# Kernel optimization log

Hardware: AMD Instinct MI355X
Metric: run time of the kernel (lower is better)

The kernel has to match this reference:

```python
import jax, jax.numpy as jnp
import numpy as np

LMAX = 3

def make_i2l(lmax):
    # [(lmax+1)^2, lmax+1] 0/1 indicator mapping irrep index -> degree l
    i2l = np.zeros(((lmax + 1) ** 2, lmax + 1), dtype=np.float32)
    count = 0
    for l in range(lmax + 1):
        i2l[count:count + 2 * l + 1, l] = 1.0
        count += 2 * l + 1
    return jnp.asarray(i2l)

def setup_inputs() -> dict:
    key = jax.random.key(0)
    x = jax.random.normal(key, (32, 512, 16, 128), dtype=jnp.float32)  # [b, n, irrep, c]
    i2l = make_i2l(LMAX)
    return {"x": x, "i2l": i2l}

def reference(x, i2l):
    # degree-wise squared norm per neighbor: [b, n, l, c]
    dot = x * x
    ll2 = jnp.einsum('bnic,il->bnlc', dot, i2l)
    # argmax over neighbors, keepdim -> [b, 1, l, c]
    idx = jnp.argmax(ll2, axis=1, keepdims=True)
    # broadcast degree-wise winner index back to irrep components: [b, 1, irrep, c]
    idx_i = jnp.einsum('belc,il->beic', idx.astype(x.dtype), i2l).astype(jnp.int32)
    # gather winning neighbor per (irrep, channel), squeeze neighbor dim -> [b, irrep, c]
    out = jnp.take_along_axis(x, idx_i, axis=1)[:, 0]
    return out
```

## Files before the change

kernel.cpp:

```cpp
#include <hip/hip_runtime.h>
#include <stdint.h>


constexpr int B_  = 32;
constexpr int N_  = 512;
constexpr int IR_ = 16;
constexpr int C_  = 128;
constexpr int NL_ = 4;

constexpr int NCHUNK = 32;
constexpr int CHN    = N_ / NCHUNK;
constexpr int NROW   = 4;
constexpr int NN     = CHN / NROW;

__device__ constexpr int L_OF_I[16] = {0, 1,1,1, 2,2,2,2,2, 3,3,3,3,3,3,3};

__global__ __launch_bounds__(128)
void cmp_phase1(const float* __restrict__ x, unsigned long long* __restrict__ ws) {
    const int t    = threadIdx.x;
    const int c4   = t & 31;
    const int nrow = t >> 5;
    const int chunk = blockIdx.x;
    const int b     = blockIdx.y;

    unsigned long long best[NL_][4];
#pragma unroll
    for (int l = 0; l < NL_; ++l)
#pragma unroll
        for (int j = 0; j < 4; ++j) best[l][j] = 0ull;

    const int n0 = chunk * CHN + nrow * NN;
    const float4* __restrict__ x4 = (const float4*)x;

    for (int nn = 0; nn < NN; ++nn) {
        const int n = n0 + nn;
        const long base = ((long)(b * N_ + n) * IR_) * 32 + c4;

        float4 acc[NL_];
#pragma unroll
        for (int l = 0; l < NL_; ++l) { acc[l].x = acc[l].y = acc[l].z = acc[l].w = 0.f; }

#pragma unroll
        for (int i = 0; i < IR_; ++i) {
            const float4 v = x4[base + i * 32];
            const int l = L_OF_I[i];
            acc[l].x += v.x * v.x;
            acc[l].y += v.y * v.y;
            acc[l].z += v.z * v.z;
            acc[l].w += v.w * v.w;
        }

        const unsigned long long code = (unsigned long long)(~(unsigned int)n);
#pragma unroll
        for (int l = 0; l < NL_; ++l) {
            const float vals[4] = {acc[l].x, acc[l].y, acc[l].z, acc[l].w};
#pragma unroll
            for (int j = 0; j < 4; ++j) {
                const unsigned long long p =
                    ((unsigned long long)__float_as_uint(vals[j]) << 32) | code;
                if (p > best[l][j]) best[l][j] = p;
            }
        }
    }

    __shared__ unsigned long long red[NROW][NL_ * C_];
#pragma unroll
    for (int l = 0; l < NL_; ++l)
#pragma unroll
        for (int j = 0; j < 4; ++j)
            red[nrow][l * C_ + c4 * 4 + j] = best[l][j];
    __syncthreads();

#pragma unroll
    for (int k = 0; k < 4; ++k) {
        const int e = t + k * 128;
        unsigned long long m = red[0][e];
#pragma unroll
        for (int nr = 1; nr < NROW; ++nr) {
            const unsigned long long v = red[nr][e];
            if (v > m) m = v;
        }
        atomicMax(&ws[(long)b * (NL_ * C_) + e], m);
    }
}

__global__ __launch_bounds__(128)
void cmp_phase2(const float* __restrict__ x,
                const unsigned long long* __restrict__ ws,
                float* __restrict__ out) {
    const int c = threadIdx.x;
    const int b = blockIdx.x;

    int n_l[NL_];
#pragma unroll
    for (int l = 0; l < NL_; ++l) {
        const unsigned long long p = ws[(long)b * (NL_ * C_) + l * C_ + c];
        n_l[l] = (int)(~(unsigned int)(p & 0xFFFFFFFFull));
    }

#pragma unroll
    for (int i = 0; i < IR_; ++i) {
        const int n = n_l[L_OF_I[i]];
        out[((long)b * IR_ + i) * C_ + c] = x[(((long)b * N_ + n) * IR_ + i) * C_ + c];
    }
}

extern "C" void kernel_launch(void* const* d_in, const int* in_sizes, int n_in,
                              void* d_out, int out_size, void* d_ws, size_t ws_size,
                              hipStream_t stream) {
    const float* x = (const float*)d_in[0];
    unsigned long long* ws = (unsigned long long*)d_ws;
    float* out = (float*)d_out;

    hipMemsetAsync(d_ws, 0, (size_t)B_ * NL_ * C_ * sizeof(unsigned long long), stream);

    dim3 g1(NCHUNK, B_);
    cmp_phase1<<<g1, 128, 0, stream>>>(x, ws);
    cmp_phase2<<<B_, 128, 0, stream>>>(x, ws, out);
}
```

Before: 191.0 us.

## Replace global atomicMax and memset with per-chunk partials reduced in phase2

Phase1 now writes each chunk's packed (value,index) maxima to its own slice of the workspace instead of doing global atomicMax, so the hipMemsetAsync launch is no longer needed. Phase2 is split over (batch, degree) blocks, reduces the 32 chunk partials per element, and copies only the irreps belonging to that degree. The inner neighbor loop of phase1 is also fully unrolled. In exchange, the workspace grows by a factor of 32 and phase2 must read all of those partials.

```diff
diff --git a/kernel.cpp b/kernel.cpp
--- a/kernel.cpp
+++ b/kernel.cpp
@@ -7,6 +7,7 @@
 constexpr int IR_ = 16;
 constexpr int C_  = 128;
 constexpr int NL_ = 4;
+constexpr int E_  = NL_ * C_;
 
 constexpr int NCHUNK = 32;
 constexpr int CHN    = N_ / NCHUNK;
@@ -14,6 +15,8 @@
 constexpr int NN     = CHN / NROW;
 
 __device__ constexpr int L_OF_I[16] = {0, 1,1,1, 2,2,2,2,2, 3,3,3,3,3,3,3};
+__device__ constexpr int I0_OF_L[4] = {0, 1, 4, 9};
+__device__ constexpr int NI_OF_L[4] = {1, 3, 5, 7};
 
 __global__ __launch_bounds__(128)
 void cmp_phase1(const float* __restrict__ x, unsigned long long* __restrict__ ws) {
@@ -32,6 +35,7 @@
     const int n0 = chunk * CHN + nrow * NN;
     const float4* __restrict__ x4 = (const float4*)x;
 
+#pragma unroll
     for (int nn = 0; nn < NN; ++nn) {
         const int n = n0 + nn;
         const long base = ((long)(b * N_ + n) * IR_) * 32 + c4;
@@ -63,7 +67,7 @@
         }
     }
 
-    __shared__ unsigned long long red[NROW][NL_ * C_];
+    __shared__ unsigned long long red[NROW][E_];
 #pragma unroll
     for (int l = 0; l < NL_; ++l)
 #pragma unroll
@@ -71,6 +75,7 @@
             red[nrow][l * C_ + c4 * 4 + j] = best[l][j];
     __syncthreads();
 
+    unsigned long long* __restrict__ wsp = ws + ((long)chunk * B_ + b) * E_;
 #pragma unroll
     for (int k = 0; k < 4; ++k) {
         const int e = t + k * 128;
@@ -80,7 +85,7 @@
             const unsigned long long v = red[nr][e];
             if (v > m) m = v;
         }
-        atomicMax(&ws[(long)b * (NL_ * C_) + e], m);
+        wsp[e] = m;
     }
 }
 
@@ -90,18 +95,24 @@
                 float* __restrict__ out) {
     const int c = threadIdx.x;
     const int b = blockIdx.x;
+    const int l = blockIdx.y;
+    const int e = l * C_ + c;
 
-    int n_l[NL_];
+    unsigned long long m = 0ull;
 #pragma unroll
-    for (int l = 0; l < NL_; ++l) {
-        const unsigned long long p = ws[(long)b * (NL_ * C_) + l * C_ + c];
-        n_l[l] = (int)(~(unsigned int)(p & 0xFFFFFFFFull));
+    for (int chunk = 0; chunk < NCHUNK; ++chunk) {
+        const unsigned long long v = ws[((long)chunk * B_ + b) * E_ + e];
+        if (v > m) m = v;
     }
+    const int n = (int)(~(unsigned int)(m & 0xFFFFFFFFull));
 
-#pragma unroll
-    for (int i = 0; i < IR_; ++i) {
-        const int n = n_l[L_OF_I[i]];
-        out[((long)b * IR_ + i) * C_ + c] = x[(((long)b * N_ + n) * IR_ + i) * C_ + c];
+    const int i0 = I0_OF_L[l];
+    const int ni = NI_OF_L[l];
+    const long src = (((long)b * N_ + n) * IR_ + i0) * C_ + c;
+    const long dst = ((long)b * IR_ + i0) * C_ + c;
+#pragma unroll 7
+    for (int k = 0; k < ni; ++k) {
+        out[dst + (long)k * C_] = x[src + (long)k * C_];
     }
 }
 
@@ -112,9 +123,8 @@
     unsigned long long* ws = (unsigned long long*)d_ws;
     float* out = (float*)d_out;
 
-    hipMemsetAsync(d_ws, 0, (size_t)B_ * NL_ * C_ * sizeof(unsigned long long), stream);
-
     dim3 g1(NCHUNK, B_);
     cmp_phase1<<<g1, 128, 0, stream>>>(x, ws);
-    cmp_phase2<<<B_, 128, 0, stream>>>(x, ws, out);
+    dim3 g2(B_, NL_);
+    cmp_phase2<<<g2, 128, 0, stream>>>(x, ws, out);
 }
```

New measurement: 188.8 us, median of 2. Within noise of the previous version (-1.1%).

## Fuse argmax and gather into one kernel split by channel groups

Applied to the files above, without the earlier changes.

Replaces the memset plus two-kernel scheme (partial argmax with global atomicMax, then gather) with one kernel per (batch, 16-channel group). Each block scans all 512 neighbors for its channels, reduces with wave shuffles and shared memory, then gathers the winners directly. This removes the memset, the atomics and the second launch. The cost is that each thread now reads only a 64-byte contiguous slice per row, so global reads are less coalesced, and the grid is 256 blocks.

```diff
diff --git a/kernel.cpp b/kernel.cpp
--- a/kernel.cpp
+++ b/kernel.cpp
@@ -8,20 +8,24 @@
 constexpr int C_  = 128;
 constexpr int NL_ = 4;
 
-constexpr int NCHUNK = 32;
-constexpr int CHN    = N_ / NCHUNK;
-constexpr int NROW   = 4;
-constexpr int NN     = CHN / NROW;
+constexpr int CG_ = 8;
+constexpr int CW_ = C_ / CG_;
+constexpr int NROW = 64;
+constexpr int KN   = N_ / NROW;
 
 __device__ constexpr int L_OF_I[16] = {0, 1,1,1, 2,2,2,2,2, 3,3,3,3,3,3,3};
 
-__global__ __launch_bounds__(128)
-void cmp_phase1(const float* __restrict__ x, unsigned long long* __restrict__ ws) {
+__global__ __launch_bounds__(256)
+void cmp_fused(const float* __restrict__ x, float* __restrict__ out) {
     const int t    = threadIdx.x;
-    const int c4   = t & 31;
-    const int nrow = t >> 5;
-    const int chunk = blockIdx.x;
-    const int b     = blockIdx.y;
+    const int c4   = t & 3;
+    const int nrow = t >> 2;
+    const int wv   = t >> 6;
+    const int b    = blockIdx.x;
+    const int cg   = blockIdx.y;
+
+    const unsigned colf4 = (unsigned)(cg * 4 + c4);
+    const float4* __restrict__ x4 = (const float4*)x;
 
     unsigned long long best[NL_][4];
 #pragma unroll
@@ -29,12 +33,9 @@
 #pragma unroll
         for (int j = 0; j < 4; ++j) best[l][j] = 0ull;
 
-    const int n0 = chunk * CHN + nrow * NN;
-    const float4* __restrict__ x4 = (const float4*)x;
-
-    for (int nn = 0; nn < NN; ++nn) {
-        const int n = n0 + nn;
-        const long base = ((long)(b * N_ + n) * IR_) * 32 + c4;
+    for (int k = 0; k < KN; ++k) {
+        const int n = nrow + k * NROW;
+        const unsigned base = ((unsigned)(b * N_ + n) * IR_) * 32u + colf4;
 
         float4 acc[NL_];
 #pragma unroll
@@ -63,58 +64,53 @@
         }
     }
 
-    __shared__ unsigned long long red[NROW][NL_ * C_];
 #pragma unroll
     for (int l = 0; l < NL_; ++l)
 #pragma unroll
-        for (int j = 0; j < 4; ++j)
-            red[nrow][l * C_ + c4 * 4 + j] = best[l][j];
+        for (int j = 0; j < 4; ++j) {
+#pragma unroll
+            for (int m = 4; m < 64; m <<= 1) {
+                const unsigned long long q = __shfl_xor(best[l][j], m, 64);
+                if (q > best[l][j]) best[l][j] = q;
+            }
+        }
+
+    __shared__ unsigned long long red[4][NL_ * CW_];
+    __shared__ int nwin[NL_ * CW_];
+    if ((t & 63) < 4) {
+#pragma unroll
+        for (int l = 0; l < NL_; ++l)
+#pragma unroll
+            for (int j = 0; j < 4; ++j)
+                red[wv][l * CW_ + c4 * 4 + j] = best[l][j];
+    }
     __syncthreads();
 
+    if (t < NL_ * CW_) {
+        unsigned long long m = red[0][t];
 #pragma unroll
-    for (int k = 0; k < 4; ++k) {
-        const int e = t + k * 128;
-        unsigned long long m = red[0][e];
-#pragma unroll
-        for (int nr = 1; nr < NROW; ++nr) {
-            const unsigned long long v = red[nr][e];
+        for (int w = 1; w < 4; ++w) {
+            const unsigned long long v = red[w][t];
             if (v > m) m = v;
         }
-        atomicMax(&ws[(long)b * (NL_ * C_) + e], m);
+        nwin[t] = (int)(~(unsigned int)(m & 0xFFFFFFFFull));
     }
-}
+    __syncthreads();
 
-__global__ __launch_bounds__(128)
-void cmp_phase2(const float* __restrict__ x,
-                const unsigned long long* __restrict__ ws,
-                float* __restrict__ out) {
-    const int c = threadIdx.x;
-    const int b = blockIdx.x;
-
-    int n_l[NL_];
-#pragma unroll
-    for (int l = 0; l < NL_; ++l) {
-        const unsigned long long p = ws[(long)b * (NL_ * C_) + l * C_ + c];
-        n_l[l] = (int)(~(unsigned int)(p & 0xFFFFFFFFull));
-    }
-
-#pragma unroll
-    for (int i = 0; i < IR_; ++i) {
-        const int n = n_l[L_OF_I[i]];
-        out[((long)b * IR_ + i) * C_ + c] = x[(((long)b * N_ + n) * IR_ + i) * C_ + c];
-    }
+    const int i  = t >> 4;
+    const int ch = t & 15;
+    const int n  = nwin[L_OF_I[i] * CW_ + ch];
+    const int c  = cg * CW_ + ch;
+    out[((b * IR_) + i) * C_ + c] = x[(((unsigned)(b * N_ + n) * IR_) + i) * C_ + c];
 }
 
 extern "C" void kernel_launch(void* const* d_in, const int* in_sizes, int n_in,
                               void* d_out, int out_size, void* d_ws, size_t ws_size,
                               hipStream_t stream) {
     const float* x = (const float*)d_in[0];
-    unsigned long long* ws = (unsigned long long*)d_ws;
     float* out = (float*)d_out;
+    (void)d_ws; (void)ws_size;
 
-    hipMemsetAsync(d_ws, 0, (size_t)B_ * NL_ * C_ * sizeof(unsigned long long), stream);
-
-    dim3 g1(NCHUNK, B_);
-    cmp_phase1<<<g1, 128, 0, stream>>>(x, ws);
-    cmp_phase2<<<B_, 128, 0, stream>>>(x, ws, out);
+    dim3 g(B_, CG_);
+    cmp_fused<<<g, 256, 0, stream>>>(x, out);
 }
```

Result: slower. 211.8 us (+10.9%).
